# Kernel tuning notes

Measured on AMD Instinct MI355X. Metric: run time of the kernel, lower is better.

Reference implementation:

```python
import jax, jax.numpy as jnp
import numpy as np

B, N, DIN, DH, DOUT, H = 2, 512, 32, 64, 64, 4
NEG_SLOPE = 0.2  # PyG GATv2Conv default
EPS = 1e-5       # LayerNorm eps


def layernorm(y, g, b):
    mu = jnp.mean(y, axis=-1, keepdims=True)
    var = jnp.mean(jnp.square(y - mu), axis=-1, keepdims=True)
    return (y - mu) * jax.lax.rsqrt(var + EPS) * g + b


def gatv2(x, wl, bl, wr, br, att, bias, mask):
    """Dense GATv2 over all-pairs edges given boolean mask [N,N] (j->i)."""
    Bb, Nn, _ = x.shape
    Hh, Dd = att.shape
    xl = (x @ wl + bl).reshape(Bb, Nn, Hh, Dd)  # source features W_l x_j
    xr = (x @ wr + br).reshape(Bb, Nn, Hh, Dd)  # target features W_r x_i
    # e[b,h,i,j] = att_h . leaky_relu(xl[b,j,h] + xr[b,i,h])
    z = jax.nn.leaky_relu(xl[:, None, :, :, :] + xr[:, :, None, :, :], NEG_SLOPE)  # [B,i,j,H,D]
    e = jnp.einsum('bijhd,hd->bhij', z, att)
    e = jnp.where(mask[None, None], e, -jnp.inf)
    alpha = jax.nn.softmax(e, axis=-1)            # softmax over source j per target i
    out = jnp.einsum('bhij,bjhd->bihd', alpha, xl).reshape(Bb, Nn, Hh * Dd)
    return out + bias


def setup_inputs() -> dict:
    key = jax.random.key(0)
    ks = jax.random.split(key, 10)
    s = lambda k, shape: (jax.random.normal(k, shape, dtype=jnp.float32) * 0.1)
    return {
        'x': jax.random.normal(ks[0], (B, N, DIN), dtype=jnp.float32),
        'embedding': jax.random.normal(ks[1], (N, DH), dtype=jnp.float32),
        # gat1: in_dim -> hidden_dim, 4 heads, concat
        'w1_l': s(ks[2], (DIN, H * DH)), 'b1_l': jnp.zeros((H * DH,), jnp.float32),
        'w1_r': s(ks[3], (DIN, H * DH)), 'b1_r': jnp.zeros((H * DH,), jnp.float32),
        'att1': s(ks[4], (H, DH)), 'bias1': jnp.zeros((H * DH,), jnp.float32),
        'g1': jnp.ones((H * DH,), jnp.float32), 'be1': jnp.zeros((H * DH,), jnp.float32),
        # gat2: 4*hidden_dim -> out_dim, 4 heads, concat
        'w2_l': s(ks[5], (H * DH, H * DOUT)), 'b2_l': jnp.zeros((H * DOUT,), jnp.float32),
        'w2_r': s(ks[6], (H * DH, H * DOUT)), 'b2_r': jnp.zeros((H * DOUT,), jnp.float32),
        'att2': s(ks[7], (H, DOUT)), 'bias2': jnp.zeros((H * DOUT,), jnp.float32),
        'g2': jnp.ones((H * DOUT,), jnp.float32), 'be2': jnp.zeros((H * DOUT,), jnp.float32),
    }


def reference(x, embedding, w1_l, b1_l, w1_r, b1_r, att1, bias1, g1, be1,
              w2_l, b2_l, w2_r, b2_r, att2, bias2, g2, be2):
    # AdaptiveAdjacency: cosine-similarity adjacency; only its nonzero
    # PATTERN is used (edge_index = adj.nonzero()); self-loops added by GATv2Conv.
    ne = embedding * jax.lax.rsqrt(jnp.sum(embedding * embedding, axis=1, keepdims=True))
    adj = ne @ ne.T
    mask = (adj != 0) | jnp.eye(N, dtype=bool)
    h = gatv2(x, w1_l, b1_l, w1_r, b1_r, att1, bias1, mask)
    h = jax.nn.relu(layernorm(h, g1, be1))
    # dropout(p=0.3) is identity in eval mode
    out = gatv2(h, w2_l, b2_l, w2_r, b2_r, att2, bias2, mask)
    out = layernorm(out, g2, be2)
    return out
```

## Files before the change

### kernel.cpp

```cpp
#include <hip/hip_runtime.h>


#define BB   2
#define NN   512
#define DIN  32
#define DH   64
#define HH   4
#define C1   256
#define C2   256
#define TI   8
#define NJC  4
#define LEPS 1e-5f

typedef unsigned long long u64;

__device__ __forceinline__ float bf_sum(float v) {
#pragma unroll
    for (int o = 32; o > 0; o >>= 1) v += __shfl_xor(v, o, 64);
    return v;
}

__device__ __forceinline__ void gload_lds16(const float* g, float* l) {
    __builtin_amdgcn_global_load_lds(
        (const __attribute__((address_space(1))) void*)g,
        (__attribute__((address_space(3))) void*)l, 16, 0, 0);
}

__global__ __launch_bounds__(256) void mask_k(const float* __restrict__ emb,
                                              u64* __restrict__ mask64) {
    __shared__ __align__(16) float s_ei[16][DH];
    __shared__ float ebuf[64][DH + 1];
    int it = blockIdx.x, jq = blockIdx.y;
    int t = threadIdx.x, lane = t & 63, iq = t >> 6;
    int j0 = jq * 64;
    {
        int row = t >> 4, d4 = (t & 15) << 2;
        *(float4*)&s_ei[row][d4] = *(const float4*)(emb + (it * 16 + row) * DH + d4);
    }
#pragma unroll
    for (int k = 0; k < 4; k++) {
        int idx = k * 256 + t, jl = idx >> 4, d4 = (idx & 15) << 2;
        float4 v = *(const float4*)(emb + (j0 + jl) * DH + d4);
        ebuf[jl][d4] = v.x; ebuf[jl][d4 + 1] = v.y;
        ebuf[jl][d4 + 2] = v.z; ebuf[jl][d4 + 3] = v.w;
    }
    __syncthreads();
    float acc[4] = {0.f, 0.f, 0.f, 0.f};
    for (int dc = 0; dc < 16; dc++) {
        int d = dc * 4;
        float e0 = ebuf[lane][d], e1 = ebuf[lane][d + 1];
        float e2 = ebuf[lane][d + 2], e3 = ebuf[lane][d + 3];
#pragma unroll
        for (int r = 0; r < 4; r++) {
            float4 iv = *(const float4*)&s_ei[iq * 4 + r][d];
            acc[r] += iv.x * e0 + iv.y * e1 + iv.z * e2 + iv.w * e3;
        }
    }
    int jg = j0 + lane;
#pragma unroll
    for (int r = 0; r < 4; r++) {
        int ig = it * 16 + iq * 4 + r;
        u64 bal = __ballot(acc[r] != 0.f || ig == jg);
        if (lane == 0) mask64[ig * 8 + jq] = bal;
    }
}

__global__ __launch_bounds__(256) void proj1_k(const float* __restrict__ x,
        const float* __restrict__ wl, const float* __restrict__ bl,
        const float* __restrict__ wr, const float* __restrict__ br,
        const float* __restrict__ att,
        float* __restrict__ xl, float* __restrict__ xr,
        float* __restrict__ sl, float* __restrict__ sr) {
    __shared__ float s_x[4][DIN];
    int t = threadIdx.x, lane = t & 63, row0 = blockIdx.x * 4, cq = blockIdx.y;
    if (t < 128) s_x[t >> 5][t & 31] = x[(row0 + (t >> 5)) * DIN + (t & 31)];
    __syncthreads();
    int cl = t & 127, half = t >> 7;
    int gc = cq * 128 + cl;
    const float* wbase; float bias; float* obase; float* sdst; int oc;
    if (gc < C1) { wbase = wl + gc; bias = bl[gc]; obase = xl; sdst = sl; oc = gc; }
    else         { wbase = wr + gc - C1; bias = br[gc - C1]; obase = xr; sdst = sr; oc = gc - C1; }
    int ra = half * 2, rb = ra + 1;
    float a0 = bias, a1 = bias;
#pragma unroll
    for (int k = 0; k < DIN; k++) {
        float wv = wbase[(size_t)k * C1];
        a0 += s_x[ra][k] * wv;
        a1 += s_x[rb][k] * wv;
    }
    obase[(size_t)(row0 + ra) * C1 + oc] = a0;
    obase[(size_t)(row0 + rb) * C1 + oc] = a1;
    float attv = att[oc];
    float s0 = bf_sum(attv * a0) * 0.6f;
    float s1 = bf_sum(attv * a1) * 0.6f;
    if (lane == 0) {
        int h = oc >> 6;
        int rwa = row0 + ra, rwb = row0 + rb;
        sdst[(h * BB + (rwa >> 9)) * NN + (rwa & 511)] = s0;
        sdst[(h * BB + (rwb >> 9)) * NN + (rwb & 511)] = s1;
    }
}

__global__ __launch_bounds__(256) void projln_k(const float* __restrict__ pagg,
        const float* __restrict__ plsum, const float* __restrict__ abias,
        const float* __restrict__ g, const float* __restrict__ be,
        const float* __restrict__ wl, const float* __restrict__ bl,
        const float* __restrict__ wr, const float* __restrict__ br,
        const float* __restrict__ att,
        float* __restrict__ xl, float* __restrict__ xr,
        float* __restrict__ sl, float* __restrict__ sr) {
    __shared__ __align__(16) float s_h[4][C1];
    int t = threadIdx.x, lane = t & 63, w = t >> 6;
    int row0 = blockIdx.x * 4, cq = blockIdx.y;
    {
        int rgb = row0 + w;
        int bb = rgb >> 9, ii = rgb & 511;
        int c4 = lane << 2, hh = lane >> 4;
        float vx = 0.f, vy = 0.f, vz = 0.f, vw = 0.f, l = 0.f;
#pragma unroll
        for (int jc = 0; jc < NJC; jc++) {
            float4 a = *(const float4*)(pagg + ((size_t)jc * BB * NN + rgb) * C1 + c4);
            vx += a.x; vy += a.y; vz += a.z; vw += a.w;
            l += plsum[((size_t)jc * HH * BB + hh * BB + bb) * NN + ii];
        }
        float inv = 1.f / l;
        float4 bi = *(const float4*)(abias + c4);
        vx = vx * inv + bi.x; vy = vy * inv + bi.y;
        vz = vz * inv + bi.z; vw = vw * inv + bi.w;
        float mu = bf_sum(vx + vy + vz + vw) * (1.f / 256.f);
        float dx = vx - mu, dy = vy - mu, dz = vz - mu, dw = vw - mu;
        float var = bf_sum(dx * dx + dy * dy + dz * dz + dw * dw) * (1.f / 256.f);
        float rs = rsqrtf(var + LEPS);
        float4 gv = *(const float4*)(g + c4);
        float4 bv = *(const float4*)(be + c4);
        float4 y;
        y.x = fmaxf(dx * rs * gv.x + bv.x, 0.f);
        y.y = fmaxf(dy * rs * gv.y + bv.y, 0.f);
        y.z = fmaxf(dz * rs * gv.z + bv.z, 0.f);
        y.w = fmaxf(dw * rs * gv.w + bv.w, 0.f);
        *(float4*)&s_h[w][c4] = y;
    }
    __syncthreads();
    int cl = t & 127, half = t >> 7;
    int gc = cq * 128 + cl;
    const float* wbase; float bias; float* obase; float* sdst; int oc;
    if (gc < C2) { wbase = wl + gc; bias = bl[gc]; obase = xl; sdst = sl; oc = gc; }
    else         { wbase = wr + gc - C2; bias = br[gc - C2]; obase = xr; sdst = sr; oc = gc - C2; }
    int ra = half * 2, rb = ra + 1;
    float a0 = bias, a1 = bias;
#pragma unroll 8
    for (int k = 0; k < C1; k++) {
        float wv = wbase[(size_t)k * C2];
        a0 += s_h[ra][k] * wv;
        a1 += s_h[rb][k] * wv;
    }
    obase[(size_t)(row0 + ra) * C2 + oc] = a0;
    obase[(size_t)(row0 + rb) * C2 + oc] = a1;
    float attv = att[oc];
    float s0 = bf_sum(attv * a0) * 0.6f;
    float s1 = bf_sum(attv * a1) * 0.6f;
    if (lane == 0) {
        int h = oc >> 6;
        int rwa = row0 + ra, rwb = row0 + rb;
        sdst[(h * BB + (rwa >> 9)) * NN + (rwa & 511)] = s0;
        sdst[(h * BB + (rwb >> 9)) * NN + (rwb & 511)] = s1;
    }
}

__global__ __launch_bounds__(256) void attn_k(const float* __restrict__ xl,
        const float* __restrict__ xr, const float* __restrict__ att,
        const u64* __restrict__ mask64,
        const float* __restrict__ sl, const float* __restrict__ sr,
        float* __restrict__ pagg, float* __restrict__ plsum) {
    __shared__ __align__(16) float xbuf[128 * 64];
    __shared__ __align__(16) float s_xr[TI][DH];
    __shared__ __align__(16) float s_att[DH];
    __shared__ __align__(16) float s_p[TI][128];
    __shared__ __align__(16) float s_sl[128];
    __shared__ float s_sr[TI];
    __shared__ u64 s_m64[TI * 2];

    int bx = blockIdx.x;
    int it = bx >> 2, jc = bx & 3;
    int h = blockIdx.y, b = blockIdx.z;
    int t = threadIdx.x, lane = t & 63, w = t >> 6;
    int i0 = it * TI, j0 = jc * 128;
    int w2 = w * 2;

    const float* xlbase = xl + (size_t)b * NN * C1 + h * DH;

    {
        int jr0 = w * 32;
#pragma unroll
        for (int k = 0; k < 8; k++) {
            int jrow = jr0 + k * 4 + (lane >> 4);
            int dslot = (lane & 15) ^ (jrow & 7);
            const float* gp = xlbase + (size_t)(j0 + jrow) * C1 + (dslot << 2);
            gload_lds16(gp, &xbuf[(jr0 + k * 4) * 64]);
        }
    }
    if (t < TI * 16) {
        int row = t >> 4, d4 = (t & 15) << 2;
        *(float4*)&s_xr[row][d4] =
            *(const float4*)(xr + (size_t)(b * NN + i0 + row) * C1 + h * DH + d4);
    }
    if (t < DH) s_att[t] = att[h * DH + t] * 0.4f;
    if (t < TI) s_sr[t] = sr[(h * BB + b) * NN + i0 + t];
    if (t < TI * 2) s_m64[t] = mask64[(i0 + (t >> 1)) * 8 + jc * 2 + (t & 1)];
    if (t < 32) *(float4*)&s_sl[t << 2] = *(const float4*)(sl + (h * BB + b) * NN + j0 + (t << 2));
    __syncthreads();

    float rsr0 = s_sr[w2], rsr1 = s_sr[w2 + 1];
    int swz = lane & 7;

    float acc00 = 0.f, acc01 = 0.f, acc10 = 0.f, acc11 = 0.f;
#pragma unroll 4
    for (int dc = 0; dc < 16; dc++) {
        float4 av  = *(const float4*)&s_att[dc << 2];
        float4 rv0 = *(const float4*)&s_xr[w2][dc << 2];
        float4 rv1 = *(const float4*)&s_xr[w2 + 1][dc << 2];
        int so = (dc ^ swz) << 2;
        float4 xv0 = *(const float4*)&xbuf[lane * 64 + so];
        float4 xv1 = *(const float4*)&xbuf[(64 + lane) * 64 + so];
        acc00 = fmaf(av.x, fabsf(xv0.x + rv0.x), acc00);
        acc00 = fmaf(av.y, fabsf(xv0.y + rv0.y), acc00);
        acc00 = fmaf(av.z, fabsf(xv0.z + rv0.z), acc00);
        acc00 = fmaf(av.w, fabsf(xv0.w + rv0.w), acc00);
        acc01 = fmaf(av.x, fabsf(xv0.x + rv1.x), acc01);
        acc01 = fmaf(av.y, fabsf(xv0.y + rv1.y), acc01);
        acc01 = fmaf(av.z, fabsf(xv0.z + rv1.z), acc01);
        acc01 = fmaf(av.w, fabsf(xv0.w + rv1.w), acc01);
        acc10 = fmaf(av.x, fabsf(xv1.x + rv0.x), acc10);
        acc10 = fmaf(av.y, fabsf(xv1.y + rv0.y), acc10);
        acc10 = fmaf(av.z, fabsf(xv1.z + rv0.z), acc10);
        acc10 = fmaf(av.w, fabsf(xv1.w + rv0.w), acc10);
        acc11 = fmaf(av.x, fabsf(xv1.x + rv1.x), acc11);
        acc11 = fmaf(av.y, fabsf(xv1.y + rv1.y), acc11);
        acc11 = fmaf(av.z, fabsf(xv1.z + rv1.z), acc11);
        acc11 = fmaf(av.w, fabsf(xv1.w + rv1.w), acc11);
    }

    float slv0 = s_sl[lane], slv1 = s_sl[64 + lane];
    u64 m0a = s_m64[w2 * 2 + 0],       m0b = s_m64[w2 * 2 + 1];
    u64 m1a = s_m64[(w2 + 1) * 2 + 0], m1b = s_m64[(w2 + 1) * 2 + 1];
    float p00 = ((m0a >> lane) & 1ull) ? __expf(slv0 + rsr0 + acc00) : 0.f;
    float p01 = ((m1a >> lane) & 1ull) ? __expf(slv0 + rsr1 + acc01) : 0.f;
    float p10 = ((m0b >> lane) & 1ull) ? __expf(slv1 + rsr0 + acc10) : 0.f;
    float p11 = ((m1b >> lane) & 1ull) ? __expf(slv1 + rsr1 + acc11) : 0.f;
    s_p[w2][lane]          = p00;
    s_p[w2 + 1][lane]      = p01;
    s_p[w2][64 + lane]     = p10;
    s_p[w2 + 1][64 + lane] = p11;
    float lsum0 = p00 + p10;
    float lsum1 = p01 + p11;
    __threadfence_block();

    int l2 = lane >> 2, lm = lane & 3;
    int off[8];
#pragma unroll
    for (int v = 0; v < 8; v++) off[v] = (((l2 ^ v) << 2) | lm);

    float agg0 = 0.f, agg1 = 0.f;
#pragma unroll 2
    for (int j8 = 0; j8 < 16; j8++) {
        int rb = j8 * 512;
        float4 pa0 = *(const float4*)&s_p[w2][j8 * 8];
        float4 pb0 = *(const float4*)&s_p[w2][j8 * 8 + 4];
        float4 pa1 = *(const float4*)&s_p[w2 + 1][j8 * 8];
        float4 pb1 = *(const float4*)&s_p[w2 + 1][j8 * 8 + 4];
        float x0 = xbuf[rb +   0 + off[0]];
        float x1 = xbuf[rb +  64 + off[1]];
        float x2 = xbuf[rb + 128 + off[2]];
        float x3 = xbuf[rb + 192 + off[3]];
        float x4 = xbuf[rb + 256 + off[4]];
        float x5 = xbuf[rb + 320 + off[5]];
        float x6 = xbuf[rb + 384 + off[6]];
        float x7 = xbuf[rb + 448 + off[7]];
        agg0 += pa0.x * x0 + pa0.y * x1 + pa0.z * x2 + pa0.w * x3
              + pb0.x * x4 + pb0.y * x5 + pb0.z * x6 + pb0.w * x7;
        agg1 += pa1.x * x0 + pa1.y * x1 + pa1.z * x2 + pa1.w * x3
              + pb1.x * x4 + pb1.y * x5 + pb1.z * x6 + pb1.w * x7;
    }

    float l0 = bf_sum(lsum0), l1 = bf_sum(lsum1);
    size_t orow = ((size_t)jc * BB * NN + b * NN + i0 + w2) * C1 + h * DH + lane;
    pagg[orow] = agg0;
    pagg[orow + C1] = agg1;
    if (lane == 0) {
        plsum[((size_t)jc * HH * BB + h * BB + b) * NN + i0 + w2] = l0;
        plsum[((size_t)jc * HH * BB + h * BB + b) * NN + i0 + w2 + 1] = l1;
    }
}

__global__ __launch_bounds__(256) void ln2_k(const float* __restrict__ pagg,
        const float* __restrict__ plsum, const float* __restrict__ abias,
        const float* __restrict__ g, const float* __restrict__ be,
        float* __restrict__ outp) {
    int t = threadIdx.x, lane = t & 63, w = t >> 6;
    int rgb = blockIdx.x * 4 + w;
    int bb = rgb >> 9, ii = rgb & 511;
    int c4 = lane << 2, hh = lane >> 4;
    float vx = 0.f, vy = 0.f, vz = 0.f, vw = 0.f, l = 0.f;
#pragma unroll
    for (int jc = 0; jc < NJC; jc++) {
        float4 a = *(const float4*)(pagg + ((size_t)jc * BB * NN + rgb) * C1 + c4);
        vx += a.x; vy += a.y; vz += a.z; vw += a.w;
        l += plsum[((size_t)jc * HH * BB + hh * BB + bb) * NN + ii];
    }
    float inv = 1.f / l;
    float4 bi = *(const float4*)(abias + c4);
    vx = vx * inv + bi.x; vy = vy * inv + bi.y;
    vz = vz * inv + bi.z; vw = vw * inv + bi.w;
    float mu = bf_sum(vx + vy + vz + vw) * (1.f / 256.f);
    float dx = vx - mu, dy = vy - mu, dz = vz - mu, dw = vw - mu;
    float var = bf_sum(dx * dx + dy * dy + dz * dz + dw * dw) * (1.f / 256.f);
    float rs = rsqrtf(var + LEPS);
    float4 gv = *(const float4*)(g + c4);
    float4 bv = *(const float4*)(be + c4);
    float4 y;
    y.x = dx * rs * gv.x + bv.x;
    y.y = dy * rs * gv.y + bv.y;
    y.z = dz * rs * gv.z + bv.z;
    y.w = dw * rs * gv.w + bv.w;
    *(float4*)(outp + (size_t)rgb * C1 + c4) = y;
}

extern "C" void kernel_launch(void* const* d_in, const int* in_sizes, int n_in,
                              void* d_out, int out_size, void* d_ws, size_t ws_size,
                              hipStream_t stream) {
    const float* x    = (const float*)d_in[0];
    const float* emb  = (const float*)d_in[1];
    const float* w1l  = (const float*)d_in[2];
    const float* b1l  = (const float*)d_in[3];
    const float* w1r  = (const float*)d_in[4];
    const float* b1r  = (const float*)d_in[5];
    const float* att1 = (const float*)d_in[6];
    const float* bia1 = (const float*)d_in[7];
    const float* g1   = (const float*)d_in[8];
    const float* be1  = (const float*)d_in[9];
    const float* w2l  = (const float*)d_in[10];
    const float* b2l  = (const float*)d_in[11];
    const float* w2r  = (const float*)d_in[12];
    const float* b2r  = (const float*)d_in[13];
    const float* att2 = (const float*)d_in[14];
    const float* bia2 = (const float*)d_in[15];
    const float* g2   = (const float*)d_in[16];
    const float* be2  = (const float*)d_in[17];

    char* w = (char*)d_ws;
    float* xl    = (float*)w; w += (size_t)BB * NN * C1 * 4;
    float* xr    = (float*)w; w += (size_t)BB * NN * C1 * 4;
    float* pagg  = (float*)w; w += (size_t)NJC * BB * NN * C1 * 4;
    u64* mask64  = (u64*)w;   w += (size_t)NN * 8 * 8;
    float* plsum = (float*)w; w += (size_t)NJC * HH * BB * NN * 4;
    float* sl    = (float*)w; w += (size_t)HH * BB * NN * 4;
    float* sr    = (float*)w; w += (size_t)HH * BB * NN * 4;

    mask_k<<<dim3(NN / 16, 8), 256, 0, stream>>>(emb, mask64);
    proj1_k<<<dim3(BB * NN / 4, 4), 256, 0, stream>>>(x, w1l, b1l, w1r, b1r, att1, xl, xr, sl, sr);
    attn_k<<<dim3((NN / TI) * NJC, HH, BB), 256, 0, stream>>>(xl, xr, att1, mask64, sl, sr, pagg, plsum);
    projln_k<<<dim3(BB * NN / 4, 4), 256, 0, stream>>>(pagg, plsum, bia1, g1, be1,
                                                       w2l, b2l, w2r, b2r, att2, xl, xr, sl, sr);
    attn_k<<<dim3((NN / TI) * NJC, HH, BB), 256, 0, stream>>>(xl, xr, att2, mask64, sl, sr, pagg, plsum);
    ln2_k<<<BB * NN / 4, 256, 0, stream>>>(pagg, plsum, bia2, g2, be2, (float*)d_out);
}
```

Baseline: 162.6 us.

## Broadcast attention weights via wave shuffles instead of LDS in aggregation

Drops the shared-memory buffer for softmax numerators and instead broadcasts per-source weights with wave shuffles. Each lane now reads float4 vectors of source features from LDS and accumulates four output channels across a quarter of the sources, followed by a cross-quarter shuffle reduction and float4 stores from a subset of lanes. The aim is fewer LDS reads and wider loads in the aggregation loop, at the cost of more shuffle instructions and a final reduction.

```diff
diff --git a/kernel.cpp b/kernel.cpp
--- a/kernel.cpp
+++ b/kernel.cpp
@@ -175,7 +175,6 @@
     __shared__ __align__(16) float xbuf[128 * 64];
     __shared__ __align__(16) float s_xr[TI][DH];
     __shared__ __align__(16) float s_att[DH];
-    __shared__ __align__(16) float s_p[TI][128];
     __shared__ __align__(16) float s_sl[128];
     __shared__ float s_sr[TI];
     __shared__ u64 s_m64[TI * 2];
@@ -247,45 +246,48 @@
     float p01 = ((m1a >> lane) & 1ull) ? __expf(slv0 + rsr1 + acc01) : 0.f;
     float p10 = ((m0b >> lane) & 1ull) ? __expf(slv1 + rsr0 + acc10) : 0.f;
     float p11 = ((m1b >> lane) & 1ull) ? __expf(slv1 + rsr1 + acc11) : 0.f;
-    s_p[w2][lane]          = p00;
-    s_p[w2 + 1][lane]      = p01;
-    s_p[w2][64 + lane]     = p10;
-    s_p[w2 + 1][64 + lane] = p11;
     float lsum0 = p00 + p10;
     float lsum1 = p01 + p11;
-    __threadfence_block();
-
-    int l2 = lane >> 2, lm = lane & 3;
-    int off[8];
-#pragma unroll
-    for (int v = 0; v < 8; v++) off[v] = (((l2 ^ v) << 2) | lm);
-
-    float agg0 = 0.f, agg1 = 0.f;
-#pragma unroll 2
+
+    int q = lane >> 4, c16 = lane & 15;
+    const float* be_ = &xbuf[q * 64 + ((c16 ^ q) << 2)];
+    const float* bo_ = &xbuf[q * 64 + ((c16 ^ q ^ 4) << 2)];
+    float4 a0 = {0.f, 0.f, 0.f, 0.f}, a1 = {0.f, 0.f, 0.f, 0.f};
+#pragma unroll
     for (int j8 = 0; j8 < 16; j8++) {
-        int rb = j8 * 512;
-        float4 pa0 = *(const float4*)&s_p[w2][j8 * 8];
-        float4 pb0 = *(const float4*)&s_p[w2][j8 * 8 + 4];
-        float4 pa1 = *(const float4*)&s_p[w2 + 1][j8 * 8];
-        float4 pb1 = *(const float4*)&s_p[w2 + 1][j8 * 8 + 4];
-        float x0 = xbuf[rb +   0 + off[0]];
-        float x1 = xbuf[rb +  64 + off[1]];
-        float x2 = xbuf[rb + 128 + off[2]];
-        float x3 = xbuf[rb + 192 + off[3]];
-        float x4 = xbuf[rb + 256 + off[4]];
-        float x5 = xbuf[rb + 320 + off[5]];
-        float x6 = xbuf[rb + 384 + off[6]];
-        float x7 = xbuf[rb + 448 + off[7]];
-        agg0 += pa0.x * x0 + pa0.y * x1 + pa0.z * x2 + pa0.w * x3
-              + pb0.x * x4 + pb0.y * x5 + pb0.z * x6 + pb0.w * x7;
-        agg1 += pa1.x * x0 + pa1.y * x1 + pa1.z * x2 + pa1.w * x3
-              + pb1.x * x4 + pb1.y * x5 + pb1.z * x6 + pb1.w * x7;
+        const float* bp = (j8 & 1) ? bo_ : be_;
+        float4 xv = *(const float4*)(bp + j8 * 256);
+        int sj = j8 * 4 + q;
+        float pr0 = __shfl(p00, sj, 64);
+        float pr1 = __shfl(p01, sj, 64);
+        a0.x += pr0 * xv.x; a0.y += pr0 * xv.y; a0.z += pr0 * xv.z; a0.w += pr0 * xv.w;
+        a1.x += pr1 * xv.x; a1.y += pr1 * xv.y; a1.z += pr1 * xv.z; a1.w += pr1 * xv.w;
+    }
+#pragma unroll
+    for (int j8 = 16; j8 < 32; j8++) {
+        const float* bp = (j8 & 1) ? bo_ : be_;
+        float4 xv = *(const float4*)(bp + j8 * 256);
+        int sj = (j8 - 16) * 4 + q;
+        float pr0 = __shfl(p10, sj, 64);
+        float pr1 = __shfl(p11, sj, 64);
+        a0.x += pr0 * xv.x; a0.y += pr0 * xv.y; a0.z += pr0 * xv.z; a0.w += pr0 * xv.w;
+        a1.x += pr1 * xv.x; a1.y += pr1 * xv.y; a1.z += pr1 * xv.z; a1.w += pr1 * xv.w;
+    }
+#pragma unroll
+    for (int o = 16; o <= 32; o <<= 1) {
+        a0.x += __shfl_xor(a0.x, o, 64); a0.y += __shfl_xor(a0.y, o, 64);
+        a0.z += __shfl_xor(a0.z, o, 64); a0.w += __shfl_xor(a0.w, o, 64);
+        a1.x += __shfl_xor(a1.x, o, 64); a1.y += __shfl_xor(a1.y, o, 64);
+        a1.z += __shfl_xor(a1.z, o, 64); a1.w += __shfl_xor(a1.w, o, 64);
     }
 
     float l0 = bf_sum(lsum0), l1 = bf_sum(lsum1);
-    size_t orow = ((size_t)jc * BB * NN + b * NN + i0 + w2) * C1 + h * DH + lane;
-    pagg[orow] = agg0;
-    pagg[orow + C1] = agg1;
+    size_t obase = ((size_t)jc * BB * NN + b * NN + i0 + w2) * C1 + h * DH;
+    if (lane < 16) {
+        *(float4*)&pagg[obase + (c16 << 2)] = a0;
+    } else if (lane < 32) {
+        *(float4*)&pagg[obase + C1 + (c16 << 2)] = a1;
+    }
     if (lane == 0) {
         plsum[((size_t)jc * HH * BB + h * BB + b) * NN + i0 + w2] = l0;
         plsum[((size_t)jc * HH * BB + h * BB + b) * NN + i0 + w2 + 1] = l1;
```

New measurement: 162.3 us. About the same (-0.2%).
